# Kernel optimization log

Hardware: AMD Instinct MI355X
Metric: run time of the kernel (lower is better)

## Reference

```python
import jax, jax.numpy as jnp
import numpy as np

OUT_H = 7
OUT_W = 7
RATIO = 2  # sampling_ratio (static)


def _roi_align(feat, boxes, out_h, out_w, sx, sy, ratio):
    """torchvision-style RoIAlign (aligned=False) on a single image.
    feat: [C,H,W], boxes: [N,4] (x1,y1,x2,y2) in image coords.
    sx, sy: spatial scales (W_feat/W_img, H_feat/H_img). Returns [N,C,out_h,out_w]."""
    C, H, W = feat.shape
    N = boxes.shape[0]
    x1 = boxes[:, 0] * sx
    y1 = boxes[:, 1] * sy
    x2 = boxes[:, 2] * sx
    y2 = boxes[:, 3] * sy
    rw = jnp.maximum(x2 - x1, 1.0)
    rh = jnp.maximum(y2 - y1, 1.0)
    bw = rw / out_w
    bh = rh / out_h
    offs = (jnp.arange(ratio, dtype=feat.dtype) + 0.5) / ratio  # sub-bin sample offsets
    # sample coordinates: [N, out*ratio]
    gy = y1[:, None, None] + (jnp.arange(out_h, dtype=feat.dtype)[None, :, None] + offs[None, None, :]) * bh[:, None, None]
    gx = x1[:, None, None] + (jnp.arange(out_w, dtype=feat.dtype)[None, :, None] + offs[None, None, :]) * bw[:, None, None]
    Y = gy.reshape(N, out_h * ratio)
    X = gx.reshape(N, out_w * ratio)
    vy = (Y >= -1.0) & (Y <= H)
    vx = (X >= -1.0) & (X <= W)
    Yc = jnp.clip(Y, 0.0, H - 1)
    Xc = jnp.clip(X, 0.0, W - 1)
    y0 = jnp.floor(Yc).astype(jnp.int32)
    x0 = jnp.floor(Xc).astype(jnp.int32)
    y1i = jnp.minimum(y0 + 1, H - 1)
    x1i = jnp.minimum(x0 + 1, W - 1)
    ly = Yc - y0.astype(Yc.dtype)
    lx = Xc - x0.astype(Xc.dtype)
    hy = 1.0 - ly
    hx = 1.0 - lx

    def g(yi, xi):  # corner gather -> [C, N, out_h*ratio, out_w*ratio]
        return feat[:, yi[:, :, None], xi[:, None, :]]

    val = (hy[:, :, None] * hx[:, None, :]) * g(y0, x0) \
        + (hy[:, :, None] * lx[:, None, :]) * g(y0, x1i) \
        + (ly[:, :, None] * hx[:, None, :]) * g(y1i, x0) \
        + (ly[:, :, None] * lx[:, None, :]) * g(y1i, x1i)
    valid = vy[:, :, None] & vx[:, None, :]
    val = jnp.where(valid[None], val, 0.0)
    # average over the ratio x ratio sampling grid (always divide by ratio^2)
    val = val.reshape(C, N, out_h, ratio, out_w, ratio).mean(axis=(3, 5))
    return val.transpose(1, 0, 2, 3)


def setup_inputs() -> dict:
    key = jax.random.key(0)
    k0, k1, k2, kb = jax.random.split(key, 4)
    img_h, img_w = 800, 1216
    feat0 = jax.random.normal(k0, (1, 256, 200, 304), dtype=jnp.float32)
    feat1 = jax.random.normal(k1, (1, 256, 100, 152), dtype=jnp.float32)
    feat2 = jax.random.normal(k2, (1, 256, 50, 76), dtype=jnp.float32)
    u = jax.random.uniform(kb, (256, 4), dtype=jnp.float32)
    bx1 = u[:, 0] * (img_w - 32)
    by1 = u[:, 1] * (img_h - 32)
    bw = 16.0 + u[:, 2] * 256.0
    bh = 16.0 + u[:, 3] * 256.0
    bx2 = jnp.minimum(bx1 + bw, float(img_w))
    by2 = jnp.minimum(by1 + bh, float(img_h))
    boxes = jnp.stack([bx1, by1, bx2, by2], axis=1)
    return {"feat0": feat0, "feat1": feat1, "feat2": feat2, "boxes": boxes,
            "img_h": img_h, "img_w": img_w}


def reference(feat0, feat1, feat2, boxes, img_h, img_w):
    _, C, H, W = feat0.shape
    # upsample coarser levels by 2**i, half-pixel bilinear == torch align_corners=False
    ups = [feat0]
    for i, f in enumerate([feat1, feat2], 1):
        s = 2 ** i
        ups.append(jax.image.resize(
            f, (f.shape[0], f.shape[1], f.shape[2] * s, f.shape[3] * s), method='bilinear'))
    fused = jnp.concatenate(ups, axis=1)[0]  # [3C, H, W] (single image)
    sx = W / img_w
    sy = H / img_h
    return _roi_align(fused, boxes, OUT_H, OUT_W, sx, sy, RATIO)
```

## Files before the change

### kernel.cpp

```cpp
#include <hip/hip_runtime.h>
#include <hip/hip_fp16.h>

#define H0 200
#define W0 304
#define H1 100
#define W1 152
#define H2 50
#define W2 76
#define CPL 256
#define CTOT 768
#define OH 7
#define OW 7
#define NPOS 49
#define CBLK 128
#define SROWP 131

#define P0 (H0*W0)
#define P1 (H1*W1)
#define P2 (H2*W2)
#define T0_OFF ((size_t)0)
#define T1_OFF ((size_t)P0*CPL)
#define T2_OFF ((size_t)P0*CPL + (size_t)P1*CPL)
#define WS_ELEMS ((size_t)P0*CPL + (size_t)P1*CPL + (size_t)P2*CPL)
#define WS_BYTES (WS_ELEMS * 2)

__device__ __forceinline__ float hat01(float d) {
    return fmaxf(0.0f, 1.0f - fabsf(d));
}

__device__ __forceinline__ unsigned short f2h_rne(float x) {
    return __half_as_ushort(__float2half_rn(x));
}

__global__ void __launch_bounds__(256)
transpose_all_kernel(const float* __restrict__ f0, const float* __restrict__ f1,
                     const float* __restrict__ f2,
                     unsigned short* __restrict__ T0,
                     unsigned short* __restrict__ T1,
                     unsigned short* __restrict__ T2, int n0, int n01) {
    __shared__ unsigned short tile[64][72];
    int b = blockIdx.x;
    const float* in; unsigned short* outp; int P; int rel;
    if (b < n0)       { in = f0; outp = T0; P = P0; rel = b; }
    else if (b < n01) { in = f1; outp = T1; P = P1; rel = b - n0; }
    else              { in = f2; outp = T2; P = P2; rel = b - n01; }
    int p0 = (rel >> 2) * 64;
    int c0 = (rel & 3) * 64;

    int q = threadIdx.x & 15;
    int r = threadIdx.x >> 4;
    bool full = (p0 + 64 <= P);
#pragma unroll
    for (int i = 0; i < 4; ++i) {
        int c = c0 + r + 16 * i;
        int p = p0 + 4 * q;
        float4 v;
        if (full) {
            v = *(const float4*)(in + (size_t)c * P + p);
        } else {
            v.x = (p + 0 < P) ? in[(size_t)c * P + p + 0] : 0.0f;
            v.y = (p + 1 < P) ? in[(size_t)c * P + p + 1] : 0.0f;
            v.z = (p + 2 < P) ? in[(size_t)c * P + p + 2] : 0.0f;
            v.w = (p + 3 < P) ? in[(size_t)c * P + p + 3] : 0.0f;
        }
        tile[4 * q + 0][r + 16 * i] = f2h_rne(v.x);
        tile[4 * q + 1][r + 16 * i] = f2h_rne(v.y);
        tile[4 * q + 2][r + 16 * i] = f2h_rne(v.z);
        tile[4 * q + 3][r + 16 * i] = f2h_rne(v.w);
    }
    __syncthreads();
    int q8 = threadIdx.x & 7;
    int r8 = threadIdx.x >> 3;
#pragma unroll
    for (int i = 0; i < 2; ++i) {
        int p = p0 + r8 + 32 * i;
        if (p < P) {
            uint4 w = *(const uint4*)&tile[r8 + 32 * i][8 * q8];
            *(uint4*)(outp + (size_t)p * CPL + c0 + 8 * q8) = w;
        }
    }
}

template<int TY, int TX>
__device__ __forceinline__ void tap_loop(const unsigned short* __restrict__ T,
                                         const int (*__restrict__ s_idx)[6],
                                         const float (*__restrict__ s_w)[6],
                                         float (*__restrict__ sout)[SROWP],
                                         int pstart, int pcount, int col,
                                         unsigned laneByte) {
    const __half2 hz = __float2half2_rn(0.0f);
    for (int pi = 0; pi < pcount; ++pi) {
        const int pos = pstart + pi;
        const int oh = pos / 7;
        const int ow = pos - oh * 7;
        unsigned yo[TY]; float yw[TY];
#pragma unroll
        for (int j2 = 0; j2 < TY; ++j2) {
            yo[j2] = (unsigned)s_idx[oh][j2] + laneByte;
            yw[j2] = s_w[oh][j2];
        }
        unsigned xb[TX]; __half2 xw2[TX];
#pragma unroll
        for (int j2 = 0; j2 < TX; ++j2) {
            xb[j2] = (unsigned)s_idx[7 + ow][j2];
            xw2[j2] = __float2half2_rn(s_w[7 + ow][j2]);
        }

        uint4 buf[2][TX];
#pragma unroll
        for (int b = 0; b < TX; ++b) {
            unsigned vo = yo[0] + xb[b];
            asm volatile("global_load_dwordx4 %0, %1, %2"
                         : "=&v"(buf[0][b]) : "v"(vo), "s"(T));
        }
        float a0 = 0.f, a1 = 0.f, a2 = 0.f, a3 = 0.f;
        float a4 = 0.f, a5 = 0.f, a6 = 0.f, a7 = 0.f;
#pragma unroll
        for (int r = 0; r < TY; ++r) {
            if (r + 1 < TY) {
#pragma unroll
                for (int b = 0; b < TX; ++b) {
                    unsigned vo = yo[r + 1] + xb[b];
                    asm volatile("global_load_dwordx4 %0, %1, %2"
                                 : "=&v"(buf[(r + 1) & 1][b]) : "v"(vo), "s"(T));
                }
                asm volatile("s_waitcnt vmcnt(%0)" :: "n"(TX));
            } else {
                asm volatile("s_waitcnt vmcnt(0)");
            }
            __builtin_amdgcn_sched_barrier(0);
            __half2 q0 = hz, q1 = hz, q2 = hz, q3 = hz;
#pragma unroll
            for (int b = 0; b < TX; ++b) {
                const __half2 xw = xw2[b];
                const uint4 v = buf[r & 1][b];
                q0 = __hfma2(xw, *(const __half2*)&v.x, q0);
                q1 = __hfma2(xw, *(const __half2*)&v.y, q1);
                q2 = __hfma2(xw, *(const __half2*)&v.z, q2);
                q3 = __hfma2(xw, *(const __half2*)&v.w, q3);
            }
            const float wa = yw[r];
            a0 = fmaf(wa, __low2float(q0), a0);  a1 = fmaf(wa, __high2float(q0), a1);
            a2 = fmaf(wa, __low2float(q1), a2);  a3 = fmaf(wa, __high2float(q1), a3);
            a4 = fmaf(wa, __low2float(q2), a4);  a5 = fmaf(wa, __high2float(q2), a5);
            a6 = fmaf(wa, __low2float(q3), a6);  a7 = fmaf(wa, __high2float(q3), a7);
            __builtin_amdgcn_sched_barrier(0);
        }
        float4 o0, o1;
        o0.x = a0 * 0.25f; o0.y = a1 * 0.25f; o0.z = a2 * 0.25f; o0.w = a3 * 0.25f;
        o1.x = a4 * 0.25f; o1.y = a5 * 0.25f; o1.z = a6 * 0.25f; o1.w = a7 * 0.25f;
        *(float4*)(&sout[pos][col])     = o0;
        *(float4*)(&sout[pos][col + 4]) = o1;
    }
}

__global__ void __launch_bounds__(256, 5)
roi_align_cl6_kernel(const unsigned short* __restrict__ T0p,
                     const unsigned short* __restrict__ T1p,
                     const unsigned short* __restrict__ T2p,
                     const float* __restrict__ boxes,
                     const int* __restrict__ img_h_p,
                     const int* __restrict__ img_w_p,
                     float* __restrict__ out) {
    __shared__ float sout[NPOS][SROWP];
    __shared__ int   s_idx[14][6];
    __shared__ float s_w[14][6];

    const int n = blockIdx.x;
    const int j = blockIdx.y;
    const int lev = j >> 1;
    const int chalf = j & 1;
    const int tid = threadIdx.x;

    const unsigned short* T; int Hc, Wc; float inv_s;
    if (lev == 0)      { T = T0p; Hc = H0; Wc = W0; inv_s = 1.0f;  }
    else if (lev == 1) { T = T1p; Hc = H1; Wc = W1; inv_s = 0.5f;  }
    else               { T = T2p; Hc = H2; Wc = W2; inv_s = 0.25f; }

    if (tid < 14) {
        int axis = (tid >= 7) ? 1 : 0;
        int o = tid - axis * 7;
        float sx = (float)W0 / (float)img_w_p[0];
        float sy = (float)H0 / (float)img_h_p[0];
        float a1v, bs; int Hf, Hca, mul;
        if (axis) {
            a1v = boxes[n * 4 + 0] * sx;
            float a2v = boxes[n * 4 + 2] * sx;
            bs = fmaxf(a2v - a1v, 1.0f) * (1.0f / (float)OW);
            Hf = W0; Hca = Wc; mul = 1;
        } else {
            a1v = boxes[n * 4 + 1] * sy;
            float a2v = boxes[n * 4 + 3] * sy;
            bs = fmaxf(a2v - a1v, 1.0f) * (1.0f / (float)OH);
            Hf = H0; Hca = Hc; mul = Wc;
        }
        int idx[6]; float w[6];
#pragma unroll
        for (int t = 0; t < 6; ++t) { idx[t] = 0; w[t] = 0.0f; }
        if (lev == 0) {
#pragma unroll
            for (int r2 = 0; r2 < 2; ++r2) {
                float Y = a1v + ((float)o + 0.25f + 0.5f * (float)r2) * bs;
                float v = (Y >= -1.0f && Y <= (float)Hf) ? 1.0f : 0.0f;
                float Yc = fminf(fmaxf(Y, 0.0f), (float)(Hf - 1));
                int y0 = (int)Yc; float lf = Yc - (float)y0;
                idx[2 * r2]     = y0;                  w[2 * r2]     = (1.0f - lf) * v;
                idx[2 * r2 + 1] = min(y0 + 1, Hf - 1); w[2 * r2 + 1] = lf * v;
            }
        } else {
            int bases[2]; float w3[2][3];
#pragma unroll
            for (int r2 = 0; r2 < 2; ++r2) {
                float Y = a1v + ((float)o + 0.25f + 0.5f * (float)r2) * bs;
                float v = (Y >= -1.0f && Y <= (float)Hf) ? 1.0f : 0.0f;
                float Yc = fminf(fmaxf(Y, 0.0f), (float)(Hf - 1));
                int y0 = (int)Yc; float lf = Yc - (float)y0; float hf = 1.0f - lf;
                int yf1 = min(y0 + 1, Hf - 1);
                float yc0 = fminf(fmaxf(((float)y0 + 0.5f) * inv_s - 0.5f, 0.0f), (float)(Hca - 1));
                float yc1 = fminf(fmaxf(((float)yf1 + 0.5f) * inv_s - 0.5f, 0.0f), (float)(Hca - 1));
                int b2 = (int)yc0;
                bases[r2] = b2;
#pragma unroll
                for (int t2 = 0; t2 < 3; ++t2) {
                    float j2 = (float)(b2 + t2);
                    w3[r2][t2] = v * (hf * hat01(yc0 - j2) + lf * hat01(yc1 - j2));
                }
            }
            int dmax = (lev == 1) ? 3 : 2;
            int d = min(max(bases[1] - bases[0], 0), dmax);
            w[0] += w3[0][0]; w[1] += w3[0][1]; w[2] += w3[0][2];
            w[d] += w3[1][0]; w[d + 1] += w3[1][1]; w[d + 2] += w3[1][2];
#pragma unroll
            for (int t = 0; t < 6; ++t) idx[t] = min(bases[0] + t, Hca - 1);
        }
#pragma unroll
        for (int t = 0; t < 6; ++t) { s_idx[tid][t] = idx[t] * mul * CPL * 2; s_w[tid][t] = w[t]; }
    }
    __syncthreads();

    const int grp = tid >> 4;
    const int l16 = tid & 15;
    const int col = l16 * 8;
    const unsigned laneByte = (unsigned)(chalf * CBLK + col) * 2u;

    const int pstart = 3 * grp;
    const int pcount = (grp == 15) ? 4 : 3;

    if (lev == 0)      tap_loop<4, 4>(T, s_idx, s_w, sout, pstart, pcount, col, laneByte);
    else if (lev == 1) tap_loop<6, 6>(T, s_idx, s_w, sout, pstart, pcount, col, laneByte);
    else               tap_loop<5, 5>(T, s_idx, s_w, sout, pstart, pcount, col, laneByte);
    __syncthreads();

    size_t obase = (size_t)n * CTOT * NPOS + (size_t)(lev * CPL + chalf * CBLK) * NPOS;
    int c = tid / NPOS;
    int p = tid - c * NPOS;
    for (int i = tid; i < CBLK * NPOS; i += 256) {
        out[obase + i] = sout[p][c];
        c += 5; p += 11;
        if (p >= NPOS) { p -= NPOS; ++c; }
    }
}

__device__ __forceinline__ void axis_w3_fb(int yf0, int Hf, int Hc, float inv_s,
                                           float lf, int& base, float* w) {
    int yf1 = min(yf0 + 1, Hf - 1);
    float hf = 1.0f - lf;
    float yc0 = fminf(fmaxf(((float)yf0 + 0.5f) * inv_s - 0.5f, 0.0f), (float)(Hc - 1));
    float yc1 = fminf(fmaxf(((float)yf1 + 0.5f) * inv_s - 0.5f, 0.0f), (float)(Hc - 1));
    base = (int)yc0;
#pragma unroll
    for (int r = 0; r < 3; ++r) {
        float j = (float)(base + r);
        w[r] = hf * hat01(yc0 - j) + lf * hat01(yc1 - j);
    }
}

__global__ void __launch_bounds__(256)
roi_align_fused_fb_kernel(const float* __restrict__ f0,
                          const float* __restrict__ f1,
                          const float* __restrict__ f2,
                          const float* __restrict__ boxes,
                          const int* __restrict__ img_h_p,
                          const int* __restrict__ img_w_p,
                          float* __restrict__ out,
                          int total) {
    int i = blockIdx.x * blockDim.x + threadIdx.x;
    if (i >= total) return;
    int ow = i % OW;
    int t = i / OW;
    int oh = t % OH; t /= OH;
    int c = t % CTOT;
    int n = t / CTOT;
    float sx = (float)W0 / (float)img_w_p[0];
    float sy = (float)H0 / (float)img_h_p[0];
    float bx1 = boxes[n * 4 + 0] * sx;
    float by1 = boxes[n * 4 + 1] * sy;
    float bw = fmaxf(boxes[n * 4 + 2] * sx - bx1, 1.0f) / OW;
    float bh = fmaxf(boxes[n * 4 + 3] * sy - by1, 1.0f) / OH;
    int level = c >> 8;
    int cl = c & (CPL - 1);
    const float* f;
    int Hc, Wc; float inv_s;
    if (level == 0)      { f = f0 + (size_t)cl * P0; Hc = H0; Wc = W0; inv_s = 1.0f;  }
    else if (level == 1) { f = f1 + (size_t)cl * P1; Hc = H1; Wc = W1; inv_s = 0.5f;  }
    else                 { f = f2 + (size_t)cl * P2; Hc = H2; Wc = W2; inv_s = 0.25f; }
    float acc = 0.0f;
#pragma unroll
    for (int ry = 0; ry < 2; ++ry) {
        float Y = by1 + ((float)oh + 0.25f + 0.5f * ry) * bh;
        bool vy = (Y >= -1.0f) && (Y <= (float)H0);
        float Yc = fminf(fmaxf(Y, 0.0f), (float)(H0 - 1));
        int y0 = (int)Yc;
        float ly = Yc - (float)y0;
#pragma unroll
        for (int rx = 0; rx < 2; ++rx) {
            float X = bx1 + ((float)ow + 0.25f + 0.5f * rx) * bw;
            bool vx = (X >= -1.0f) && (X <= (float)W0);
            float Xc = fminf(fmaxf(X, 0.0f), (float)(W0 - 1));
            int x0 = (int)Xc;
            float lx = Xc - (float)x0;
            float v;
            if (level == 0) {
                int y1i = min(y0 + 1, H0 - 1), x1i = min(x0 + 1, W0 - 1);
                float hy = 1.0f - ly, hx = 1.0f - lx;
                float v00 = f[y0 * W0 + x0],  v01 = f[y0 * W0 + x1i];
                float v10 = f[y1i * W0 + x0], v11 = f[y1i * W0 + x1i];
                v = hy * (hx * v00 + lx * v01) + ly * (hx * v10 + lx * v11);
            } else {
                int yb, xb; float wy[3], wxl[3];
                axis_w3_fb(y0, H0, Hc, inv_s, ly, yb, wy);
                axis_w3_fb(x0, W0, Wc, inv_s, lx, xb, wxl);
                v = 0.0f;
#pragma unroll
                for (int a = 0; a < 3; ++a) {
                    int row = min(yb + a, Hc - 1) * Wc;
                    float s = 0.0f;
#pragma unroll
                    for (int b = 0; b < 3; ++b)
                        s += wxl[b] * f[row + min(xb + b, Wc - 1)];
                    v += wy[a] * s;
                }
            }
            if (vy && vx) acc += v;
        }
    }
    out[i] = acc * 0.25f;
}

extern "C" void kernel_launch(void* const* d_in, const int* in_sizes, int n_in,
                              void* d_out, int out_size, void* d_ws, size_t ws_size,
                              hipStream_t stream) {
    const float* f0    = (const float*)d_in[0];
    const float* f1    = (const float*)d_in[1];
    const float* f2    = (const float*)d_in[2];
    const float* boxes = (const float*)d_in[3];
    const int* img_h_p = (const int*)d_in[4];
    const int* img_w_p = (const int*)d_in[5];
    float* out = (float*)d_out;
    int N = in_sizes[3] / 4;

    if (ws_size >= WS_BYTES) {
        unsigned short* ws = (unsigned short*)d_ws;
        unsigned short* T0 = ws + T0_OFF;
        unsigned short* T1 = ws + T1_OFF;
        unsigned short* T2 = ws + T2_OFF;
        int n0 = ((P0 + 63) / 64) * 4;
        int n1 = ((P1 + 63) / 64) * 4;
        int n2 = ((P2 + 63) / 64) * 4;
        transpose_all_kernel<<<n0 + n1 + n2, 256, 0, stream>>>(
            f0, f1, f2, T0, T1, T2, n0, n0 + n1);
        roi_align_cl6_kernel<<<dim3(N, 6), 256, 0, stream>>>(
            T0, T1, T2, boxes, img_h_p, img_w_p, out);
    } else {
        int total = N * CTOT * OH * OW;
        roi_align_fused_fb_kernel<<<(total + 255) / 256, 256, 0, stream>>>(
            f0, f1, f2, boxes, img_h_p, img_w_p, out, total);
    }
}
```

Before: 158.3 us.

## Use separable row-then-column tap reduction for coarse levels via shared row buffer

For pyramid levels 1 and 2, the tap evaluation becomes separable. The kernel first reduces the y taps for every distinct x column the box touches into a shared-memory row buffer, then applies the x-tap weights from shared memory. This avoids reloading the same feature columns across output positions that share x taps. Level 0 keeps the direct tap loop, with the hand-written asm prefetch pipeline replaced by plain loads. The costs are a 20KB shared buffer, lower launch-bounds occupancy (3 instead of 5), extra barriers per output row, and silent clamping when a box spans more than 40 columns.

```diff
diff --git a/kernel.cpp b/kernel.cpp
--- a/kernel.cpp
+++ b/kernel.cpp
@@ -14,6 +14,7 @@
 #define NPOS 49
 #define CBLK 128
 #define SROWP 131
+#define UXMAX 40
 
 #define P0 (H0*W0)
 #define P1 (H1*W1)
@@ -81,59 +82,39 @@
     }
 }
 
-template<int TY, int TX>
-__device__ __forceinline__ void tap_loop(const unsigned short* __restrict__ T,
-                                         const int (*__restrict__ s_idx)[6],
-                                         const float (*__restrict__ s_w)[6],
-                                         float (*__restrict__ sout)[SROWP],
-                                         int pstart, int pcount, int col,
-                                         unsigned laneByte) {
+__device__ __forceinline__ void tap_loop_l0(const unsigned short* __restrict__ T,
+                                            const int (*__restrict__ s_idx)[6],
+                                            const float (*__restrict__ s_w)[6],
+                                            float (*__restrict__ sout)[SROWP],
+                                            int pstart, int pcount, int col,
+                                            unsigned laneByte) {
+    const char* Tb = (const char*)T;
     const __half2 hz = __float2half2_rn(0.0f);
     for (int pi = 0; pi < pcount; ++pi) {
         const int pos = pstart + pi;
         const int oh = pos / 7;
         const int ow = pos - oh * 7;
-        unsigned yo[TY]; float yw[TY];
-#pragma unroll
-        for (int j2 = 0; j2 < TY; ++j2) {
-            yo[j2] = (unsigned)s_idx[oh][j2] + laneByte;
+        unsigned yb[4]; float yw[4];
+#pragma unroll
+        for (int j2 = 0; j2 < 4; ++j2) {
+            yb[j2] = (unsigned)s_idx[oh][j2] + laneByte;
             yw[j2] = s_w[oh][j2];
         }
-        unsigned xb[TX]; __half2 xw2[TX];
-#pragma unroll
-        for (int j2 = 0; j2 < TX; ++j2) {
+        unsigned xb[4]; __half2 xw2[4];
+#pragma unroll
+        for (int j2 = 0; j2 < 4; ++j2) {
             xb[j2] = (unsigned)s_idx[7 + ow][j2];
             xw2[j2] = __float2half2_rn(s_w[7 + ow][j2]);
         }
-
-        uint4 buf[2][TX];
-#pragma unroll
-        for (int b = 0; b < TX; ++b) {
-            unsigned vo = yo[0] + xb[b];
-            asm volatile("global_load_dwordx4 %0, %1, %2"
-                         : "=&v"(buf[0][b]) : "v"(vo), "s"(T));
-        }
         float a0 = 0.f, a1 = 0.f, a2 = 0.f, a3 = 0.f;
         float a4 = 0.f, a5 = 0.f, a6 = 0.f, a7 = 0.f;
 #pragma unroll
-        for (int r = 0; r < TY; ++r) {
-            if (r + 1 < TY) {
-#pragma unroll
-                for (int b = 0; b < TX; ++b) {
-                    unsigned vo = yo[r + 1] + xb[b];
-                    asm volatile("global_load_dwordx4 %0, %1, %2"
-                                 : "=&v"(buf[(r + 1) & 1][b]) : "v"(vo), "s"(T));
-                }
-                asm volatile("s_waitcnt vmcnt(%0)" :: "n"(TX));
-            } else {
-                asm volatile("s_waitcnt vmcnt(0)");
-            }
-            __builtin_amdgcn_sched_barrier(0);
+        for (int r = 0; r < 4; ++r) {
             __half2 q0 = hz, q1 = hz, q2 = hz, q3 = hz;
 #pragma unroll
-            for (int b = 0; b < TX; ++b) {
+            for (int b = 0; b < 4; ++b) {
+                uint4 v = *(const uint4*)(Tb + (yb[r] + xb[b]));
                 const __half2 xw = xw2[b];
-                const uint4 v = buf[r & 1][b];
                 q0 = __hfma2(xw, *(const __half2*)&v.x, q0);
                 q1 = __hfma2(xw, *(const __half2*)&v.y, q1);
                 q2 = __hfma2(xw, *(const __half2*)&v.z, q2);
@@ -144,7 +125,6 @@
             a2 = fmaf(wa, __low2float(q1), a2);  a3 = fmaf(wa, __high2float(q1), a3);
             a4 = fmaf(wa, __low2float(q2), a4);  a5 = fmaf(wa, __high2float(q2), a5);
             a6 = fmaf(wa, __low2float(q3), a6);  a7 = fmaf(wa, __high2float(q3), a7);
-            __builtin_amdgcn_sched_barrier(0);
         }
         float4 o0, o1;
         o0.x = a0 * 0.25f; o0.y = a1 * 0.25f; o0.z = a2 * 0.25f; o0.w = a3 * 0.25f;
@@ -154,8 +134,74 @@
     }
 }
 
-__global__ void __launch_bounds__(256, 5)
-roi_align_cl6_kernel(const unsigned short* __restrict__ T0p,
+template<int TT>
+__device__ __forceinline__ void sep_level(const unsigned short* __restrict__ T,
+                                          const int (*__restrict__ s_idx)[6],
+                                          const float (*__restrict__ s_w)[6],
+                                          float (*__restrict__ sout)[SROWP],
+                                          float* __restrict__ rowbuf,
+                                          int tid, unsigned chalfByte) {
+    int xloB = s_idx[7][0], xhiB = xloB;
+#pragma unroll
+    for (int o = 0; o < 7; ++o) {
+#pragma unroll
+        for (int t = 0; t < TT; ++t) {
+            int v = s_idx[7 + o][t];
+            xloB = min(xloB, v);
+            xhiB = max(xhiB, v);
+        }
+    }
+    const int ux = ((xhiB - xloB) >> 9) + 1;
+    const int g = tid >> 4;
+    const int l16 = tid & 15;
+    const char* Tbase = (const char*)T + chalfByte + (unsigned)(l16 * 16) + (unsigned)xloB;
+
+    for (int oh = 0; oh < OH; ++oh) {
+        for (int s = g; s < ux; s += 16) {
+            const char* bp = Tbase + ((unsigned)s << 9);
+            float a0 = 0.f, a1 = 0.f, a2 = 0.f, a3 = 0.f;
+            float a4 = 0.f, a5 = 0.f, a6 = 0.f, a7 = 0.f;
+#pragma unroll
+            for (int t = 0; t < TT; ++t) {
+                uint4 v = *(const uint4*)(bp + (unsigned)s_idx[oh][t]);
+                const float wy = s_w[oh][t];
+                float2 f0 = __half22float2(*(const __half2*)&v.x);
+                float2 f1 = __half22float2(*(const __half2*)&v.y);
+                float2 f2 = __half22float2(*(const __half2*)&v.z);
+                float2 f3 = __half22float2(*(const __half2*)&v.w);
+                a0 = fmaf(wy, f0.x, a0); a1 = fmaf(wy, f0.y, a1);
+                a2 = fmaf(wy, f1.x, a2); a3 = fmaf(wy, f1.y, a3);
+                a4 = fmaf(wy, f2.x, a4); a5 = fmaf(wy, f2.y, a5);
+                a6 = fmaf(wy, f3.x, a6); a7 = fmaf(wy, f3.y, a7);
+            }
+            float4* rp = (float4*)&rowbuf[s * CBLK + l16 * 8];
+            rp[0] = make_float4(a0, a1, a2, a3);
+            rp[1] = make_float4(a4, a5, a6, a7);
+        }
+        __syncthreads();
+        if (tid < 224) {
+            const int ow = tid >> 5;
+            const int ch = (tid & 31) * 4;
+            float b0 = 0.f, b1 = 0.f, b2 = 0.f, b3 = 0.f;
+#pragma unroll
+            for (int t = 0; t < TT; ++t) {
+                int s = (s_idx[7 + ow][t] - xloB) >> 9;
+                s = min(s, UXMAX - 1);
+                const float wx = s_w[7 + ow][t];
+                const float4 rv = *(const float4*)&rowbuf[s * CBLK + ch];
+                b0 = fmaf(wx, rv.x, b0); b1 = fmaf(wx, rv.y, b1);
+                b2 = fmaf(wx, rv.z, b2); b3 = fmaf(wx, rv.w, b3);
+            }
+            const int pos = oh * 7 + ow;
+            *(float4*)(&sout[pos][ch]) =
+                make_float4(b0 * 0.25f, b1 * 0.25f, b2 * 0.25f, b3 * 0.25f);
+        }
+        __syncthreads();
+    }
+}
+
+__global__ void __launch_bounds__(256, 3)
+roi_align_sep_kernel(const unsigned short* __restrict__ T0p,
                      const unsigned short* __restrict__ T1p,
                      const unsigned short* __restrict__ T2p,
                      const float* __restrict__ boxes,
@@ -163,6 +209,7 @@
                      const int* __restrict__ img_w_p,
                      float* __restrict__ out) {
     __shared__ float sout[NPOS][SROWP];
+    __shared__ __align__(16) float rowbuf[UXMAX * CBLK];
     __shared__ int   s_idx[14][6];
     __shared__ float s_w[14][6];
 
@@ -238,17 +285,21 @@
     }
     __syncthreads();
 
-    const int grp = tid >> 4;
-    const int l16 = tid & 15;
-    const int col = l16 * 8;
-    const unsigned laneByte = (unsigned)(chalf * CBLK + col) * 2u;
-
-    const int pstart = 3 * grp;
-    const int pcount = (grp == 15) ? 4 : 3;
-
-    if (lev == 0)      tap_loop<4, 4>(T, s_idx, s_w, sout, pstart, pcount, col, laneByte);
-    else if (lev == 1) tap_loop<6, 6>(T, s_idx, s_w, sout, pstart, pcount, col, laneByte);
-    else               tap_loop<5, 5>(T, s_idx, s_w, sout, pstart, pcount, col, laneByte);
+    const unsigned chalfByte = (unsigned)(chalf * CBLK) * 2u;
+
+    if (lev == 0) {
+        const int grp = tid >> 4;
+        const int l16 = tid & 15;
+        const int col = l16 * 8;
+        const unsigned laneByte = chalfByte + (unsigned)col * 2u;
+        const int pstart = 3 * grp;
+        const int pcount = (grp == 15) ? 4 : 3;
+        tap_loop_l0(T, s_idx, s_w, sout, pstart, pcount, col, laneByte);
+    } else if (lev == 1) {
+        sep_level<6>(T, s_idx, s_w, sout, rowbuf, tid, chalfByte);
+    } else {
+        sep_level<5>(T, s_idx, s_w, sout, rowbuf, tid, chalfByte);
+    }
     __syncthreads();
 
     size_t obase = (size_t)n * CTOT * NPOS + (size_t)(lev * CPL + chalf * CBLK) * NPOS;
@@ -369,7 +420,7 @@
         int n2 = ((P2 + 63) / 64) * 4;
         transpose_all_kernel<<<n0 + n1 + n2, 256, 0, stream>>>(
             f0, f1, f2, T0, T1, T2, n0, n0 + n1);
-        roi_align_cl6_kernel<<<dim3(N, 6), 256, 0, stream>>>(
+        roi_align_sep_kernel<<<dim3(N, 6), 256, 0, stream>>>(
             T0, T1, T2, boxes, img_h_p, img_w_p, out);
     } else {
         int total = N * CTOT * OH * OW;
```

Result: slower. 165.4 us (+4.5%).
